# Performance work log

Hardware: AMD Instinct MI355X
Metric: run time of the kernel (lower is better)

## Reference

```python
import jax, jax.numpy as jnp
import numpy as np
from itertools import permutations

G_ORDER = 12  # tetrahedral rotation group A4


def _a4_group():
    # Even permutations of 4 elements -> A4, order 12.
    def parity(p):
        inv = sum(1 for i in range(4) for j in range(i + 1, 4) if p[i] > p[j])
        return inv % 2
    perms = [p for p in permutations(range(4)) if parity(p) == 0]
    idx = {p: i for i, p in enumerate(perms)}
    def compose(a, b):  # (a o b)[i] = a[b[i]]
        return tuple(a[b[i]] for i in range(4))
    cayley = np.zeros((G_ORDER, G_ORDER), dtype=np.int32)
    inv = np.zeros((G_ORDER,), dtype=np.int32)
    ident = tuple(range(4))
    for i, a in enumerate(perms):
        for j, b in enumerate(perms):
            cayley[i, j] = idx[compose(a, b)]
            if compose(a, b) == ident:
                inv[i] = j
    return cayley, inv


def setup_inputs() -> dict:
    key = jax.random.key(0)
    k_x, k_kernel, k_bias = jax.random.split(key, 3)
    N = 524288
    in_features = 192
    out_features = 192
    G = G_ORDER
    in_ch = in_features // G   # 16
    out_ch = out_features // G  # 16
    fan_in = G * in_ch  # variance-preserving init from the module
    std = 1.0 / np.sqrt(fan_in)
    x = jax.random.normal(k_x, (N, in_features), dtype=jnp.float32)
    kernel = jax.random.normal(k_kernel, (G, out_ch, in_ch), dtype=jnp.float32) * std
    bias = jax.random.uniform(k_bias, (out_ch,), dtype=jnp.float32, minval=-std, maxval=std)
    cayley_np, inv_np = _a4_group()
    return {
        "x": x,
        "kernel": kernel,
        "bias": bias,
        "cayley_table": jnp.asarray(cayley_np),
        "inverse_indices": jnp.asarray(inv_np),
    }


def reference(x, kernel, bias, cayley_table, inverse_indices):
    G, out_ch, in_ch = kernel.shape
    # kernel_group_idx[h, g] = cayley_table[inverse_indices[g], h]
    h = jnp.arange(G)[:, None]            # [G,1]
    inv_g = inverse_indices[None, :]      # [1,G]
    kernel_group_idx = cayley_table[inv_g, h]          # [G,G]
    expanded = kernel[kernel_group_idx]                # [G,G,O,I]
    # permute(0,2,1,3).reshape -> [G*O, G*I]
    W = jnp.transpose(expanded, (0, 2, 1, 3)).reshape(G * out_ch, G * in_ch)
    out = x @ W.T                                      # [N, G*O]
    out = out.reshape(*x.shape[:-1], G, out_ch) + bias
    return out.reshape(*x.shape[:-1], G * out_ch)
```

## Files before the change

### kernel.cpp

```cpp
#include <hip/hip_runtime.h>
#include <hip/hip_bf16.h>
#include <stdint.h>

typedef __attribute__((ext_vector_type(8))) short short8;
typedef __attribute__((ext_vector_type(4))) float f32x4;

__device__ __forceinline__ unsigned short f2bf(float f) {
    union { float f; uint32_t u; } v; v.f = f;
    return (unsigned short)((v.u + 0x7FFFu + ((v.u >> 16) & 1u)) >> 16);
}

__global__ void build_w_kernel(const float* __restrict__ kern,
                               const int* __restrict__ cayley,
                               const int* __restrict__ inv,
                               unsigned short* __restrict__ Wfrag) {
    int i = blockIdx.x * blockDim.x + threadIdx.x;
    if (i >= 192 * 192) return;
    int e    = i & 7;
    int lane = (i >> 3) & 63;
    int fc   = i >> 9;
    int ct   = fc / 6, c = fc - ct * 6;
    int j = ct * 16 + (lane & 15);
    int lhi = lane >> 4;
    int k = c * 32 + ((e < 4) ? (lhi * 4 + e) : (16 + lhi * 4 + (e - 4)));
    int h = j >> 4, oc = j & 15;
    int g = k >> 4, ic = k & 15;
    int cidx = cayley[inv[g] * 12 + h];
    Wfrag[i] = f2bf(kern[cidx * 256 + oc * 16 + ic]);
}

__global__ __launch_bounds__(256, 1) void gemm_kernel(
    const float* __restrict__ x,
    const unsigned short* __restrict__ Wfrag,
    const float* __restrict__ bias,
    float* __restrict__ out, int nstrips, int spb) {
  __shared__ unsigned char xb[16 * 784];
  __shared__ unsigned char ob[16 * 784];
  const int tid  = threadIdx.x;
  const int lane = tid & 63;
  const int wid  = tid >> 6;
  const int l15  = lane & 15;
  const int lhi  = lane >> 4;

  short8 wf[3][6];
  #pragma unroll
  for (int t = 0; t < 3; ++t)
    #pragma unroll
    for (int c = 0; c < 6; ++c)
      wf[t][c] = *(const short8*)(Wfrag + (((wid * 3 + t) * 6 + c) * 64 + lane) * 8);

  const f32x4 bias4 = *(const f32x4*)(bias + lhi * 4);

  int goff[3], coff[3];
  #pragma unroll
  for (int t = 0; t < 3; ++t) {
    int idx = ((wid * 3 + t) << 6) + lane;
    int row = idx / 48;
    int cb  = idx - row * 48;
    goff[t] = idx << 4;
    coff[t] = row * 784 + (cb << 4);
  }
  const int fbase = l15 * 784 + lhi * 16;
  int obw[3];
  #pragma unroll
  for (int t = 0; t < 3; ++t) obw[t] = l15 * 784 + (wid * 3 + t) * 64 + lhi * 16;

  int strip = blockIdx.x * spb;
  const int send = min(strip + spb, nstrips);
  if (strip >= send) return;

  f32x4 pre[3];
  {
    const unsigned char* xs = (const unsigned char*)x + (size_t)strip * 12288;
    #pragma unroll
    for (int t = 0; t < 3; ++t) pre[t] = *(const f32x4*)(xs + goff[t]);
  }

  while (strip < send) {
    #pragma unroll
    for (int t = 0; t < 3; ++t) *(f32x4*)(xb + coff[t]) = pre[t];
    __syncthreads();

    short8 abf[6];
    #pragma unroll
    for (int c = 0; c < 6; ++c) {
      f32x4 lo = *(const f32x4*)(xb + fbase + c * 128);
      f32x4 hi = *(const f32x4*)(xb + fbase + c * 128 + 64);
      short8 v;
      #pragma unroll
      for (int e = 0; e < 4; ++e) {
        v[e]     = (short)f2bf(lo[e]);
        v[e + 4] = (short)f2bf(hi[e]);
      }
      abf[c] = v;
    }

    const int nxt = strip + 1;
    if (nxt < send) {
      const unsigned char* xs = (const unsigned char*)x + (size_t)nxt * 12288;
      #pragma unroll
      for (int t = 0; t < 3; ++t) pre[t] = *(const f32x4*)(xs + goff[t]);
    }

    #pragma unroll
    for (int t = 0; t < 3; ++t) {
      f32x4 acc = {0.f, 0.f, 0.f, 0.f};
      #pragma unroll
      for (int c = 0; c < 6; ++c)
        acc = __builtin_amdgcn_mfma_f32_16x16x32_bf16(wf[t][c], abf[c], acc, 0, 0, 0);
      f32x4 res = {acc[0] + bias4[0], acc[1] + bias4[1],
                   acc[2] + bias4[2], acc[3] + bias4[3]};
      *(f32x4*)(ob + obw[t]) = res;
    }
    __syncthreads();

    {
      unsigned char* os = (unsigned char*)out + (size_t)strip * 12288;
      #pragma unroll
      for (int t = 0; t < 3; ++t) {
        f32x4 v = *(const f32x4*)(ob + coff[t]);
        *(f32x4*)(os + goff[t]) = v;
      }
    }
    __syncthreads();
    strip = nxt;
  }
}

extern "C" void kernel_launch(void* const* d_in, const int* in_sizes, int n_in,
                              void* d_out, int out_size, void* d_ws, size_t ws_size,
                              hipStream_t stream) {
    const float* x      = (const float*)d_in[0];
    const float* kern   = (const float*)d_in[1];
    const float* bias   = (const float*)d_in[2];
    const int*   cayley = (const int*)d_in[3];
    const int*   inv    = (const int*)d_in[4];
    float* out = (float*)d_out;
    unsigned short* Wfrag = (unsigned short*)d_ws;

    const int nrows = in_sizes[0] / 192;
    const int nstrips = nrows / 16;

    build_w_kernel<<<(192 * 192 + 255) / 256, 256, 0, stream>>>(kern, cayley, inv, Wfrag);

    const int nblocks = 2048;
    const int spb     = (nstrips + nblocks - 1) / nblocks;
    gemm_kernel<<<nblocks, 256, 0, stream>>>(x, Wfrag, bias, out, nstrips, spb);
}
```

Before: 168.3 us.

## Double-buffer x tiles via direct global-to-LDS loads with XOR swizzle

Replaces the register-staged prefetch of each 16-row x strip with global_load_lds DMA into a double-buffered LDS tile. The layout is XOR-swizzled to avoid bank conflicts, and manual vmcnt/lgkmcnt waits with raw barriers replace __syncthreads. The aim is to overlap the next strip's load with the current strip's compute and to drop the register-to-LDS store pass. It relies on hand-tuned waitcnt counts and a reduced barrier count, which risks ordering hazards, for example buffer reuse without a trailing barrier.

```diff
diff --git a/kernel.cpp b/kernel.cpp
--- a/kernel.cpp
+++ b/kernel.cpp
@@ -8,6 +8,12 @@
 __device__ __forceinline__ unsigned short f2bf(float f) {
     union { float f; uint32_t u; } v; v.f = f;
     return (unsigned short)((v.u + 0x7FFFu + ((v.u >> 16) & 1u)) >> 16);
+}
+
+__device__ __forceinline__ void gload16(const void* g, void* l) {
+  __builtin_amdgcn_global_load_lds(
+      (const __attribute__((address_space(1))) unsigned int*)g,
+      (__attribute__((address_space(3))) unsigned int*)l, 16, 0, 0);
 }
 
 __global__ void build_w_kernel(const float* __restrict__ kern,
@@ -34,7 +40,7 @@
     const unsigned short* __restrict__ Wfrag,
     const float* __restrict__ bias,
     float* __restrict__ out, int nstrips, int spb) {
-  __shared__ unsigned char xb[16 * 784];
+  __shared__ unsigned char xb[2][16 * 768];
   __shared__ unsigned char ob[16 * 784];
   const int tid  = threadIdx.x;
   const int lane = tid & 63;
@@ -51,41 +57,64 @@
 
   const f32x4 bias4 = *(const f32x4*)(bias + lhi * 4);
 
-  int goff[3], coff[3];
+  int gsrc[3];
   #pragma unroll
   for (int t = 0; t < 3; ++t) {
+    int L  = ((wid * 3 + t) << 6) + lane;
+    int r  = L / 48;
+    int u  = L - r * 48;
+    int ug = u ^ (r & 7);
+    gsrc[t] = r * 768 + (ug << 4);
+  }
+  int frl[6], frh[6];
+  #pragma unroll
+  for (int c = 0; c < 6; ++c) {
+    frl[c] = l15 * 768 + (((c * 8 + lhi)     ^ (l15 & 7)) << 4);
+    frh[c] = l15 * 768 + (((c * 8 + lhi + 4) ^ (l15 & 7)) << 4);
+  }
+  int obw[3], coff[3], goff[3];
+  #pragma unroll
+  for (int t = 0; t < 3; ++t) {
+    obw[t] = l15 * 784 + (wid * 3 + t) * 64 + lhi * 16;
     int idx = ((wid * 3 + t) << 6) + lane;
     int row = idx / 48;
     int cb  = idx - row * 48;
     goff[t] = idx << 4;
     coff[t] = row * 784 + (cb << 4);
   }
-  const int fbase = l15 * 784 + lhi * 16;
-  int obw[3];
-  #pragma unroll
-  for (int t = 0; t < 3; ++t) obw[t] = l15 * 784 + (wid * 3 + t) * 64 + lhi * 16;
 
-  int strip = blockIdx.x * spb;
-  const int send = min(strip + spb, nstrips);
-  if (strip >= send) return;
+  const int s0 = blockIdx.x * spb;
+  const int send = min(s0 + spb, nstrips);
+  if (s0 >= send) return;
 
-  f32x4 pre[3];
   {
-    const unsigned char* xs = (const unsigned char*)x + (size_t)strip * 12288;
+    const unsigned char* xs = (const unsigned char*)x + (size_t)s0 * 12288;
+    unsigned char* lb = xb[0] + wid * 3 * 1024;
     #pragma unroll
-    for (int t = 0; t < 3; ++t) pre[t] = *(const f32x4*)(xs + goff[t]);
+    for (int t = 0; t < 3; ++t) gload16(xs + gsrc[t], lb + t * 1024);
   }
+  __syncthreads();
 
-  while (strip < send) {
-    #pragma unroll
-    for (int t = 0; t < 3; ++t) *(f32x4*)(xb + coff[t]) = pre[t];
-    __syncthreads();
+  int cur = 0;
+  for (int s = s0; s < send; ++s) {
+    {
+      const int pf = (s + 1 < send) ? (s + 1) : (send - 1);
+      const unsigned char* xs = (const unsigned char*)x + (size_t)pf * 12288;
+      unsigned char* lb = xb[cur ^ 1] + wid * 3 * 1024;
+      #pragma unroll
+      for (int t = 0; t < 3; ++t) gload16(xs + gsrc[t], lb + t * 1024);
+    }
 
+    asm volatile("s_waitcnt vmcnt(6)" ::: "memory");
+    __builtin_amdgcn_sched_barrier(0);
+    __builtin_amdgcn_s_barrier();
+
+    const unsigned char* xcur = xb[cur];
     short8 abf[6];
     #pragma unroll
     for (int c = 0; c < 6; ++c) {
-      f32x4 lo = *(const f32x4*)(xb + fbase + c * 128);
-      f32x4 hi = *(const f32x4*)(xb + fbase + c * 128 + 64);
+      f32x4 lo = *(const f32x4*)(xcur + frl[c]);
+      f32x4 hi = *(const f32x4*)(xcur + frh[c]);
       short8 v;
       #pragma unroll
       for (int e = 0; e < 4; ++e) {
@@ -93,13 +122,6 @@
         v[e + 4] = (short)f2bf(hi[e]);
       }
       abf[c] = v;
-    }
-
-    const int nxt = strip + 1;
-    if (nxt < send) {
-      const unsigned char* xs = (const unsigned char*)x + (size_t)nxt * 12288;
-      #pragma unroll
-      for (int t = 0; t < 3; ++t) pre[t] = *(const f32x4*)(xs + goff[t]);
     }
 
     #pragma unroll
@@ -112,18 +134,18 @@
                    acc[2] + bias4[2], acc[3] + bias4[3]};
       *(f32x4*)(ob + obw[t]) = res;
     }
-    __syncthreads();
+    asm volatile("s_waitcnt lgkmcnt(0)" ::: "memory");
+    __builtin_amdgcn_s_barrier();
 
     {
-      unsigned char* os = (unsigned char*)out + (size_t)strip * 12288;
+      unsigned char* os = (unsigned char*)out + (size_t)s * 12288;
       #pragma unroll
       for (int t = 0; t < 3; ++t) {
         f32x4 v = *(const f32x4*)(ob + coff[t]);
         *(f32x4*)(os + goff[t]) = v;
       }
     }
-    __syncthreads();
-    strip = nxt;
+    cur ^= 1;
   }
 }
 
```

Measured after the change: 175.1 us. 1.04x slower.
